# Performance work log

Measured on AMD Instinct MI355X. Metric: run time of the kernel, lower is better.

## Reference

```python
import jax, jax.numpy as jnp
import numpy as np

B, S, D, H, DH = 4, 1024, 1024, 16, 64  # batch, seq, d_model, heads, head dim (d_Q=d_K=d_V)


def setup_inputs() -> dict:
    key = jax.random.key(0)
    ks = jax.random.split(key, 12)
    std = 0.02
    return {
        "x_Q": jax.random.normal(ks[0], (B, S, D), jnp.float32),
        "x_K": jax.random.normal(ks[1], (B, S, D), jnp.float32),
        "x_V": jax.random.normal(ks[2], (B, S, D), jnp.float32),
        "src_batch_lens": jax.random.randint(ks[3], (B,), 0, S),
        # stacked per-head projection weights: [H, d_model, head_dim]
        "Wq": jax.random.normal(ks[4], (H, D, DH), jnp.float32) * std,
        "bq": jax.random.normal(ks[5], (H, DH), jnp.float32) * std,
        "Wk": jax.random.normal(ks[6], (H, D, DH), jnp.float32) * std,
        "bk": jax.random.normal(ks[7], (H, DH), jnp.float32) * std,
        "Wv": jax.random.normal(ks[8], (H, D, DH), jnp.float32) * std,
        "bv": jax.random.normal(ks[9], (H, DH), jnp.float32) * std,
        "Wo": jax.random.normal(ks[10], (D, D), jnp.float32) * std,
        "bo": jax.random.normal(ks[11], (D,), jnp.float32) * std,
    }


def reference(x_Q, x_K, x_V, src_batch_lens, Wq, bq, Wk, bk, Wv, bv, Wo, bo):
    dq = Wq.shape[-1]
    seq = x_Q.shape[1]
    # all heads at once instead of the per-head python loop
    Q = jnp.einsum('bsd,hde->bhse', x_Q, Wq) + bq[None, :, None, :]
    K = jnp.einsum('bsd,hde->bhse', x_K, Wk) + bk[None, :, None, :]
    V = jnp.einsum('bsd,hde->bhse', x_V, Wv) + bv[None, :, None, :]
    scores = jnp.einsum('bhse,bhte->bhst', Q, K) / jnp.sqrt(jnp.asarray(dq, x_Q.dtype))
    # original: matmul(diag(1..1,0..0), scores) zeroes query rows >= length
    rowmask = (jnp.arange(seq)[None, :] < src_batch_lens[:, None])  # [B, S]
    scores = scores * rowmask[:, None, :, None].astype(scores.dtype)
    A = jax.nn.softmax(scores, axis=-1)  # torch Softmax(dim=2) on [B,S,S] per head = key axis
    AV = jnp.einsum('bhst,bhtv->bhsv', A, V)
    out = AV.transpose(0, 2, 1, 3).reshape(x_Q.shape[0], seq, -1)  # concat heads on dim 2
    return out @ Wo + bo  # dropout p=0 -> identity
```

## Files before the change

### kernel.cpp

```cpp
#include <hip/hip_runtime.h>
#include <stdint.h>

typedef short v8s __attribute__((ext_vector_type(8)));
typedef short v4s __attribute__((ext_vector_type(4)));
typedef float v4f __attribute__((ext_vector_type(4)));

#define AS1 __attribute__((address_space(1)))
#define AS3 __attribute__((address_space(3)))

__device__ __forceinline__ void glds16(const void* g, void* l) {
  __builtin_amdgcn_global_load_lds((const AS1 void*)g, (AS3 void*)l, 16, 0, 0);
}

__device__ __forceinline__ short f2bf(float f) {
  uint32_t u = __float_as_uint(f);
  u += 0x7fffu + ((u >> 16) & 1u);
  return (short)(u >> 16);
}

__global__ __launch_bounds__(256) void prep_kernel(
    const float* __restrict__ xQ, const float* __restrict__ xK, const float* __restrict__ xV,
    const float* __restrict__ wq, const float* __restrict__ wk, const float* __restrict__ wv,
    const float* __restrict__ wo,
    short* __restrict__ oxQ, short* __restrict__ oxK, short* __restrict__ oxV,
    short* __restrict__ oq, short* __restrict__ ok, short* __restrict__ ov,
    short* __restrict__ oo) {
  const int bid = blockIdx.x;
  const int t = threadIdx.x;
  if (bid >= 1024) {
    const int c = bid - 1024;
    const int z = c >> 12;
    const int i = (c & 4095) * 256 + t;
    const float* in = (z == 0) ? xQ : (z == 1) ? xK : xV;
    short* out      = (z == 0) ? oxQ : (z == 1) ? oxK : oxV;
    float4 v = ((const float4*)in)[i];
    short4 o = { f2bf(v.x), f2bf(v.y), f2bf(v.z), f2bf(v.w) };
    ((short4*)out)[i] = o;
    return;
  }
  __shared__ float tile[64][65];
  const float* in;
  short* out;
  int C, R, rb, cb;
  if (bid < 768) {
    const int which = bid >> 8, rem = bid & 255;
    const int slice = rem >> 4, rbi = rem & 15;
    in  = ((which == 0) ? wq : (which == 1) ? wk : wv) + (size_t)slice * 65536;
    out = ((which == 0) ? oq : (which == 1) ? ok : ov) + (size_t)slice * 65536;
    C = 64; R = 1024; rb = rbi * 64; cb = 0;
  } else {
    const int r = bid - 768;
    in = wo; out = oo;
    C = 1024; R = 1024; rb = (r >> 4) * 64; cb = (r & 15) * 64;
  }
  const int col = t & 63, r0 = t >> 6;
#pragma unroll
  for (int i = 0; i < 16; ++i) {
    int row = r0 + i * 4;
    tile[row][col] = in[(size_t)(rb + row) * C + cb + col];
  }
  __syncthreads();
#pragma unroll
  for (int i = 0; i < 16; ++i) {
    int orow = r0 + i * 4;
    out[(size_t)(cb + orow) * R + rb + col] = f2bf(tile[col][orow]);
  }
}

template <int MR>
__device__ __forceinline__ void gemm_core(const short* __restrict__ Ag,
                                          const short* __restrict__ Bg,
                                          short* As, short* Bs,
                                          v4f (&acc)[MR / 32][4]) {
  constexpr int MT = MR / 32;
  constexpr int ASZ = MR * 32;
  constexpr int BSZ = 128 * 32;
  const int tid  = threadIdx.x;
  const int lane = tid & 63;
  const int w    = tid >> 6;
  const int quad = lane >> 4;
  const int c15  = lane & 15;
  const int wr   = (w >> 1) * (MR / 2);
  const int wc   = (w & 1) * 64;

  const int r0 = tid >> 2;
  const int p0 = (tid & 3) ^ ((r0 & 3) ^ ((r0 >> 2) & 3));
  const short* a0 = Ag + (size_t)r0 * 1024 + p0 * 8;
  const short* a1 = a0 + 64 * 1024;
  const short* b0 = Bg + (size_t)r0 * 1024 + p0 * 8;
  const short* b1 = b0 + 64 * 1024;
  short* lA = As + tid * 8;
  short* lB = Bs + tid * 8;

  auto issue = [&](int t, int buf) {
    const int o = t * 32;
    glds16(a0 + o, lA + buf * ASZ);
    if constexpr (MR == 128) glds16(a1 + o, lA + buf * ASZ + 2048);
    glds16(b0 + o, lB + buf * BSZ);
    glds16(b1 + o, lB + buf * BSZ + 2048);
  };

  issue(0, 0);
  issue(1, 1);

  const int xs = (c15 & 3) ^ ((c15 >> 2) & 3);
  const int rdoff = ((quad ^ xs)) * 8;

  for (int kb = 0; kb < 32; ++kb) {
    if constexpr (MR == 128)
      asm volatile("s_waitcnt vmcnt(4)\n\ts_barrier" ::: "memory");
    else
      asm volatile("s_waitcnt vmcnt(3)\n\ts_barrier" ::: "memory");

    const int t2 = kb + 2;
    issue(t2 < 32 ? t2 : 31, t2 % 3);

    const short* Ab = As + (kb % 3) * ASZ;
    const short* Bb = Bs + (kb % 3) * BSZ;

    v8s a[MT], b[4];
#pragma unroll
    for (int mt = 0; mt < MT; ++mt)
      a[mt] = *(const v8s*)(Ab + (wr + mt * 16 + c15) * 32 + rdoff);
#pragma unroll
    for (int nt = 0; nt < 4; ++nt)
      b[nt] = *(const v8s*)(Bb + (wc + nt * 16 + c15) * 32 + rdoff);
#pragma unroll
    for (int mt = 0; mt < MT; ++mt)
#pragma unroll
      for (int nt = 0; nt < 4; ++nt)
        acc[mt][nt] = __builtin_amdgcn_mfma_f32_16x16x32_bf16(a[mt], b[nt], acc[mt][nt], 0, 0, 0);
  }
}

__global__ __launch_bounds__(256, 3) void proj_gemm(
    const short* __restrict__ xQ, const short* __restrict__ xK, const short* __restrict__ xV,
    const short* __restrict__ WqT, const short* __restrict__ WkT, const short* __restrict__ WvT,
    const float* __restrict__ bq, const float* __restrict__ bk, const float* __restrict__ bv,
    short* __restrict__ Qb, short* __restrict__ Kb, short* __restrict__ Vtb) {
  __shared__ short As[12288];
  __shared__ short Bs[12288];
  const int lin = blockIdx.x;
  const int z = lin >> 8;
  const int r = lin & 255;
  const int nb = ((r >> 3) & 7) * 128;
  const int mb = (((r & 7) << 2) + (r >> 6)) * 128;
  const short* A    = (z == 0) ? xQ  : (z == 1) ? xK  : xV;
  const short* Bt   = (z == 0) ? WqT : (z == 1) ? WkT : WvT;
  const float* bias = (z == 0) ? bq  : (z == 1) ? bk  : bv;
  short* outp       = (z == 0) ? Qb  : (z == 1) ? Kb  : Vtb;
  v4f acc[4][4] = {};
  gemm_core<128>(A + (size_t)mb * 1024, Bt + (size_t)nb * 1024, As, Bs, acc);

  const int lane = threadIdx.x & 63, w = threadIdx.x >> 6;
  const int quad = lane >> 4, c15 = lane & 15;
  const int wr = (w >> 1) * 64, wc = (w & 1) * 64;
  const bool vmode = (z == 2);
#pragma unroll
  for (int nt = 0; nt < 4; ++nt) {
    const int gn = nb + wc + nt * 16 + c15;
    const float bb = bias[gn];
    const int h = gn >> 6, e = gn & 63;
#pragma unroll
    for (int mt = 0; mt < 4; ++mt) {
      if (!vmode) {
#pragma unroll
        for (int rr = 0; rr < 4; ++rr) {
          const int gm = mb + wr + mt * 16 + quad * 4 + rr;
          const int bi = gm >> 10, s = gm & 1023;
          const size_t base = (size_t)(bi * 16 + h) * 65536;
          outp[base + (size_t)s * 64 + e] = f2bf(acc[mt][nt][rr] + bb);
        }
      } else {
        const int gm0 = mb + wr + mt * 16 + quad * 4;
        const int bi = gm0 >> 10, s0 = gm0 & 1023;
        const size_t base = (size_t)(bi * 16 + h) * 65536;
        short4 st = { f2bf(acc[mt][nt][0] + bb), f2bf(acc[mt][nt][1] + bb),
                      f2bf(acc[mt][nt][2] + bb), f2bf(acc[mt][nt][3] + bb) };
        *(short4*)&outp[base + (size_t)e * 1024 + s0] = st;
      }
    }
  }
}

__global__ __launch_bounds__(256, 3) void out_gemm(
    const short* __restrict__ AV, const short* __restrict__ WoT,
    const float* __restrict__ bo, float* __restrict__ outp) {
  __shared__ short As[6144];
  __shared__ short Bs[12288];
  const int lin = blockIdx.x;
  const int nb = ((lin >> 3) & 7) * 128;
  const int mb = (((lin & 7) << 3) + (lin >> 6)) * 64;
  v4f acc[2][4] = {};
  gemm_core<64>(AV + (size_t)mb * 1024, WoT + (size_t)nb * 1024, As, Bs, acc);
  const int lane = threadIdx.x & 63, w = threadIdx.x >> 6;
  const int quad = lane >> 4, c15 = lane & 15;
  const int wr = (w >> 1) * 32, wc = (w & 1) * 64;
#pragma unroll
  for (int nt = 0; nt < 4; ++nt) {
    const int gn = nb + wc + nt * 16 + c15;
    const float bb = bo[gn];
#pragma unroll
    for (int mt = 0; mt < 2; ++mt)
#pragma unroll
      for (int r = 0; r < 4; ++r) {
        const int gm = mb + wr + mt * 16 + quad * 4 + r;
        outp[(size_t)gm * 1024 + gn] = acc[mt][nt][r] + bb;
      }
  }
}

__global__ __launch_bounds__(256, 4) void attn_kernel(
    const short* __restrict__ Qb, const short* __restrict__ Kb,
    const short* __restrict__ Vtb, const int* __restrict__ lens,
    short* __restrict__ AVb) {
  __shared__ short Ks[2][4096];
  __shared__ short Vs[2][4096];
  const int tid = threadIdx.x, lane = tid & 63, w = tid >> 6;
  const int quad = lane >> 4, c15 = lane & 15;
  const int flat = blockIdx.x;
  const int bh = (flat & 7) + 8 * ((flat >> 3) & 7);
  const int qg = flat >> 6;
  const int b = bh >> 4, h = bh & 15;
  const short* Qp = Qb  + (size_t)bh * 65536;
  const short* Kp = Kb  + (size_t)bh * 65536;
  const short* Vp = Vtb + (size_t)bh * 65536;
  const int len = lens[b];
  const int row0 = qg * 64 + w * 16;

  v8s bq_[2];
#pragma unroll
  for (int kf = 0; kf < 2; ++kf)
    bq_[kf] = *(const v8s*)(Qp + (size_t)(row0 + c15) * 64 + kf * 32 + quad * 8);

  const float scale = (row0 + c15 < len) ? 0.125f : 0.0f;
  float sm = 0.f;
  v4f o[4] = {};

  const int srow = tid >> 3, spart = tid & 7;
  const int gpart = spart ^ (srow & 7);
  const int kgo0 = srow * 64 + gpart * 8, kgo1 = (srow + 32) * 64 + gpart * 8;
  const int vgo0 = srow * 1024 + gpart * 8, vgo1 = (srow + 32) * 1024 + gpart * 8;
  const int l0 = tid * 8, l1 = 2048 + tid * 8;

  const int c7 = c15 & 7;
  const int krow = c15 * 128;
  const int koff0 = krow + ((quad) ^ c7) * 16;
  const int koff1 = krow + ((4 + quad) ^ c7) * 16;
  const int q2 = quad >> 1, h8 = (quad & 1) * 8;
  int voff[4];
#pragma unroll
  for (int nt = 0; nt < 4; ++nt)
    voff[nt] = krow + ((2 * nt + q2) ^ c7) * 16 + h8;

  glds16(Kp + kgo0, (char*)Ks[0] + l0 * 2);
  glds16(Kp + kgo1, (char*)Ks[0] + l1 * 2);
  glds16(Vp + vgo0, (char*)Vs[0] + l0 * 2);
  glds16(Vp + vgo1, (char*)Vs[0] + l1 * 2);

  for (int kb = 0; kb < 16; ++kb) {
    const int cur = kb & 1, nxt = cur ^ 1;
    __syncthreads();

    if (kb < 15) {
      const short* kt = Kp + (size_t)(kb + 1) * 4096;
      const short* vt = Vp + (kb + 1) * 64;
      glds16(kt + kgo0, (char*)Ks[nxt] + l0 * 2);
      glds16(kt + kgo1, (char*)Ks[nxt] + l1 * 2);
      glds16(vt + vgo0, (char*)Vs[nxt] + l0 * 2);
      glds16(vt + vgo1, (char*)Vs[nxt] + l1 * 2);
    }

    v8s ak[4][2];
#pragma unroll
    for (int nt = 0; nt < 4; ++nt) {
      ak[nt][0] = *(const v8s*)((const char*)Ks[cur] + nt * 2048 + koff0);
      ak[nt][1] = *(const v8s*)((const char*)Ks[cur] + nt * 2048 + koff1);
    }

    v4f sc[4];
#pragma unroll
    for (int nt = 0; nt < 4; ++nt) {
      v4f z = {};
#pragma unroll
      for (int kf = 0; kf < 2; ++kf)
        z = __builtin_amdgcn_mfma_f32_16x16x32_bf16(ak[nt][kf], bq_[kf], z, 0, 0, 0);
      sc[nt] = z;
    }

    v4s pb[4];
#pragma unroll
    for (int nt = 0; nt < 4; ++nt) {
      v4s pv;
#pragma unroll
      for (int r = 0; r < 4; ++r) {
        float p = __expf(sc[nt][r] * scale);
        sm += p;
        pv[r] = f2bf(p);
      }
      pb[nt] = pv;
    }

    v4s av[4][4];
#pragma unroll
    for (int t = 0; t < 4; ++t)
#pragma unroll
      for (int nt = 0; nt < 4; ++nt)
        av[t][nt] = *(const v4s*)((const char*)Vs[cur] + t * 2048 + voff[nt]);

#pragma unroll
    for (int t = 0; t < 4; ++t)
#pragma unroll
      for (int nt = 0; nt < 4; ++nt)
        o[t] = __builtin_amdgcn_mfma_f32_16x16x16bf16_1k(av[t][nt], pb[nt], o[t], 0, 0, 0);
  }

  sm += __shfl_xor(sm, 16);
  sm += __shfl_xor(sm, 32);

  const float inv = 1.0f / sm;
  const size_t rowbase = (size_t)(b * 1024 + row0 + c15) * 1024 + h * 64;
#pragma unroll
  for (int t = 0; t < 4; ++t) {
    short4 st = { f2bf(o[t][0] * inv), f2bf(o[t][1] * inv),
                  f2bf(o[t][2] * inv), f2bf(o[t][3] * inv) };
    *(short4*)&AVb[rowbase + t * 16 + quad * 4] = st;
  }
}

extern "C" void kernel_launch(void* const* d_in, const int* in_sizes, int n_in,
                              void* d_out, int out_size, void* d_ws, size_t ws_size,
                              hipStream_t stream) {
  const float* xQ = (const float*)d_in[0];
  const float* xK = (const float*)d_in[1];
  const float* xV = (const float*)d_in[2];
  const int* lens = (const int*)d_in[3];
  const float* Wq = (const float*)d_in[4];
  const float* bq = (const float*)d_in[5];
  const float* Wk = (const float*)d_in[6];
  const float* bk = (const float*)d_in[7];
  const float* Wv = (const float*)d_in[8];
  const float* bv = (const float*)d_in[9];
  const float* Wo = (const float*)d_in[10];
  const float* bo = (const float*)d_in[11];
  float* out = (float*)d_out;

  char* ws = (char*)d_ws;
  short* xQb = (short*)(ws + 0);
  short* xKb = (short*)(ws + 8388608);
  short* xVb = (short*)(ws + 16777216);
  short* WqT = (short*)(ws + 25165824);
  short* WkT = (short*)(ws + 27262976);
  short* WvT = (short*)(ws + 29360128);
  short* WoT = (short*)(ws + 31457280);
  short* Qb  = (short*)(ws + 33554432);
  short* Kb  = (short*)(ws + 41943040);
  short* Vtb = (short*)(ws + 50331648);
  short* AVb = (short*)(ws + 58720256);

  prep_kernel<<<dim3(13312), 256, 0, stream>>>(xQ, xK, xV, Wq, Wk, Wv, Wo,
                                               xQb, xKb, xVb, WqT, WkT, WvT, WoT);
  proj_gemm<<<dim3(768), 256, 0, stream>>>(xQb, xKb, xVb, WqT, WkT, WvT,
                                           bq, bk, bv, Qb, Kb, Vtb);
  attn_kernel<<<dim3(1024), 256, 0, stream>>>(Qb, Kb, Vtb, lens, AVb);
  out_gemm<<<dim3(512), 256, 0, stream>>>(AVb, WoT, bo, out);
}
```

Before: 202.5 us.

## Rewrite projection GEMM with 256x256 tiles, 8 waves and double-buffered swizzled LDS

The QKV projection GEMM moves from 128x128 tiles with 4 waves to 256x256 tiles with 8 waves per block (192 blocks instead of 768). It uses double-buffered LDS with XOR-swizzled columns and K-step 64, and issues async global-to-LDS loads staged across four compute phases with explicit barriers and s_setprio around the MFMA bursts. The aim is more data reuse per byte loaded and better overlap of memory with compute. The risks are fewer blocks than CUs on the chip and higher register and LDS pressure.

New measurement: 207.5 us. +2.4%, slower.

```diff
diff --git a/kernel.cpp b/kernel.cpp
--- a/kernel.cpp
+++ b/kernel.cpp
@@ -133,46 +133,133 @@
   }
 }
 
-__global__ __launch_bounds__(256, 3) void proj_gemm(
+#define MFMA16(A, B, C) __builtin_amdgcn_mfma_f32_16x16x32_bf16(A, B, C, 0, 0, 0)
+
+__global__ __launch_bounds__(512, 2) void proj_gemm(
     const short* __restrict__ xQ, const short* __restrict__ xK, const short* __restrict__ xV,
     const short* __restrict__ WqT, const short* __restrict__ WkT, const short* __restrict__ WvT,
     const float* __restrict__ bq, const float* __restrict__ bk, const float* __restrict__ bv,
     short* __restrict__ Qb, short* __restrict__ Kb, short* __restrict__ Vtb) {
-  __shared__ short As[12288];
-  __shared__ short Bs[12288];
+  __shared__ short As_[2][16384];
+  __shared__ short Bs_[2][16384];
+
   const int lin = blockIdx.x;
-  const int z = lin >> 8;
-  const int r = lin & 255;
-  const int nb = ((r >> 3) & 7) * 128;
-  const int mb = (((r & 7) << 2) + (r >> 6)) * 128;
-  const short* A    = (z == 0) ? xQ  : (z == 1) ? xK  : xV;
-  const short* Bt   = (z == 0) ? WqT : (z == 1) ? WkT : WvT;
+  const int z = lin >> 6;
+  const int r6 = lin & 63;
+  const int tile = (r6 & 7) * 8 + (r6 >> 3);
+  const int mbase = (tile >> 2) * 256;
+  const int nbase = (tile & 3) * 256;
+
+  const short* Ag   = (z == 0) ? xQ  : (z == 1) ? xK  : xV;
+  const short* Bg   = (z == 0) ? WqT : (z == 1) ? WkT : WvT;
   const float* bias = (z == 0) ? bq  : (z == 1) ? bk  : bv;
   short* outp       = (z == 0) ? Qb  : (z == 1) ? Kb  : Vtb;
-  v4f acc[4][4] = {};
-  gemm_core<128>(A + (size_t)mb * 1024, Bt + (size_t)nb * 1024, As, Bs, acc);
-
-  const int lane = threadIdx.x & 63, w = threadIdx.x >> 6;
+
+  const int tid  = threadIdx.x;
+  const int lane = tid & 63, w = tid >> 6;
+  const int wm = w >> 2, wn = w & 3;
   const int quad = lane >> 4, c15 = lane & 15;
-  const int wr = (w >> 1) * 64, wc = (w & 1) * 64;
+  const int g3 = c15 & 7;
+  const int off0 = (quad ^ g3) * 8;
+  const int off1 = ((4 | quad) ^ g3) * 8;
+
+  const int sr = tid >> 3, sl = tid & 7;
+  const int scol = (sl ^ (sr & 7)) << 3;
+
+  auto stage = [&](int q_) {
+    if (q_ >= 128) return;
+    const int T = q_ >> 3, k = q_ & 7, bf = T & 1;
+    if (k < 4) {
+      glds16(Bg + (size_t)(nbase + k * 64 + sr) * 1024 + T * 64 + scol,
+             &Bs_[bf][k * 4096 + tid * 8]);
+    } else {
+      const int q = k - 4;
+      const int lrow = q * 32 + sr + ((sr & 32) ? 96 : 0);
+      glds16(Ag + (size_t)(mbase + lrow) * 1024 + T * 64 + scol,
+             &As_[bf][lrow * 64 + sl * 8]);
+    }
+  };
+
+  for (int i = 0; i < 11; ++i) stage(i);
+  int rq = 11;
+
+  v4f acc[8][4] = {};
+
+  asm volatile("s_waitcnt vmcnt(3)\n\ts_barrier" ::: "memory");
+
+#pragma unroll 2
+  for (int t = 0; t < 16; ++t) {
+    const short* pA = &As_[t & 1][(wm * 128 + c15) * 64];
+    const short* pB = &Bs_[t & 1][(wn * 64 + c15) * 64];
+    v8s a[2][2], b[4][2];
+
+#pragma unroll
+    for (int nf = 0; nf < 4; ++nf) {
+      b[nf][0] = *(const v8s*)(pB + nf * 1024 + off0);
+      b[nf][1] = *(const v8s*)(pB + nf * 1024 + off1);
+    }
+    a[0][0] = *(const v8s*)(pA + off0);
+    a[0][1] = *(const v8s*)(pA + off1);
+    a[1][0] = *(const v8s*)(pA + 1024 + off0);
+    a[1][1] = *(const v8s*)(pA + 1024 + off1);
+    stage(rq); stage(rq + 1); rq += 2;
+    asm volatile("s_barrier" ::: "memory");
+    __builtin_amdgcn_s_setprio(1);
+#pragma unroll
+    for (int mf = 0; mf < 2; ++mf)
+#pragma unroll
+      for (int nf = 0; nf < 4; ++nf)
+        acc[mf][nf] = MFMA16(a[mf][1], b[nf][1], MFMA16(a[mf][0], b[nf][0], acc[mf][nf]));
+    __builtin_amdgcn_s_setprio(0);
+    asm volatile("s_barrier" ::: "memory");
+
+#define PROJ_PHASE(P)                                                         \
+    a[0][0] = *(const v8s*)(pA + (P) * 2048 + off0);                          \
+    a[0][1] = *(const v8s*)(pA + (P) * 2048 + off1);                          \
+    a[1][0] = *(const v8s*)(pA + (P) * 2048 + 1024 + off0);                   \
+    a[1][1] = *(const v8s*)(pA + (P) * 2048 + 1024 + off1);                   \
+    stage(rq); stage(rq + 1); rq += 2;                                        \
+    asm volatile("s_barrier" ::: "memory");                                   \
+    __builtin_amdgcn_s_setprio(1);                                            \
+    _Pragma("unroll")                                                         \
+    for (int mf = 0; mf < 2; ++mf)                                            \
+      _Pragma("unroll")                                                       \
+      for (int nf = 0; nf < 4; ++nf)                                          \
+        acc[(P) * 2 + mf][nf] =                                               \
+            MFMA16(a[mf][1], b[nf][1],                                        \
+                   MFMA16(a[mf][0], b[nf][0], acc[(P) * 2 + mf][nf]));        \
+    __builtin_amdgcn_s_setprio(0);
+
+    PROJ_PHASE(1)
+    asm volatile("s_barrier" ::: "memory");
+    PROJ_PHASE(2)
+    asm volatile("s_barrier" ::: "memory");
+    PROJ_PHASE(3)
+    if (t < 14)
+      asm volatile("s_waitcnt vmcnt(3)\n\ts_barrier" ::: "memory");
+    else if (t == 14)
+      asm volatile("s_waitcnt vmcnt(0)\n\ts_barrier" ::: "memory");
+  }
+#undef PROJ_PHASE
+
   const bool vmode = (z == 2);
 #pragma unroll
   for (int nt = 0; nt < 4; ++nt) {
-    const int gn = nb + wc + nt * 16 + c15;
+    const int gn = nbase + wn * 64 + nt * 16 + c15;
     const float bb = bias[gn];
     const int h = gn >> 6, e = gn & 63;
 #pragma unroll
-    for (int mt = 0; mt < 4; ++mt) {
+    for (int mt = 0; mt < 8; ++mt) {
       if (!vmode) {
 #pragma unroll
         for (int rr = 0; rr < 4; ++rr) {
-          const int gm = mb + wr + mt * 16 + quad * 4 + rr;
+          const int gm = mbase + wm * 128 + mt * 16 + quad * 4 + rr;
           const int bi = gm >> 10, s = gm & 1023;
           const size_t base = (size_t)(bi * 16 + h) * 65536;
           outp[base + (size_t)s * 64 + e] = f2bf(acc[mt][nt][rr] + bb);
         }
       } else {
-        const int gm0 = mb + wr + mt * 16 + quad * 4;
+        const int gm0 = mbase + wm * 128 + mt * 16 + quad * 4;
         const int bi = gm0 >> 10, s0 = gm0 & 1023;
         const size_t base = (size_t)(bi * 16 + h) * 65536;
         short4 st = { f2bf(acc[mt][nt][0] + bb), f2bf(acc[mt][nt][1] + bb),
@@ -360,7 +447,7 @@
 
   prep_kernel<<<dim3(13312), 256, 0, stream>>>(xQ, xK, xV, Wq, Wk, Wv, Wo,
                                                xQb, xKb, xVb, WqT, WkT, WvT, WoT);
-  proj_gemm<<<dim3(768), 256, 0, stream>>>(xQb, xKb, xVb, WqT, WkT, WvT,
+  proj_gemm<<<dim3(192), 512, 0, stream>>>(xQb, xKb, xVb, WqT, WkT, WvT,
                                            bq, bk, bv, Qb, Kb, Vtb);
   attn_kernel<<<dim3(1024), 256, 0, stream>>>(Qb, Kb, Vtb, lens, AVb);
   out_gemm<<<dim3(512), 256, 0, stream>>>(AVb, WoT, bo, out);
```

## Process two query tiles per warp in attention to reuse K/V LDS fragments

Applied to the files above, without the earlier changes.

Each warp in the attention kernel now handles 32 query rows instead of 16, so every K and V fragment read from shared memory feeds two MFMA streams. Each block covers 128 query rows, and the grid is halved to 512 blocks. The intent is to cut LDS traffic and global K/V tile loads per query row. The cost is doubled accumulator and score registers, a lower occupancy target (launch bounds 2), and fewer blocks for latency hiding across the GPU's compute units.

After: 203.2 us. About the same (+0.3%).

```diff
diff --git a/kernel.cpp b/kernel.cpp
--- a/kernel.cpp
+++ b/kernel.cpp
@@ -210,7 +210,7 @@
   }
 }
 
-__global__ __launch_bounds__(256, 4) void attn_kernel(
+__global__ __launch_bounds__(256, 2) void attn_kernel(
     const short* __restrict__ Qb, const short* __restrict__ Kb,
     const short* __restrict__ Vtb, const int* __restrict__ lens,
     short* __restrict__ AVb) {
@@ -226,16 +226,20 @@
   const short* Kp = Kb  + (size_t)bh * 65536;
   const short* Vp = Vtb + (size_t)bh * 65536;
   const int len = lens[b];
-  const int row0 = qg * 64 + w * 16;
-
-  v8s bq_[2];
-#pragma unroll
-  for (int kf = 0; kf < 2; ++kf)
-    bq_[kf] = *(const v8s*)(Qp + (size_t)(row0 + c15) * 64 + kf * 32 + quad * 8);
-
-  const float scale = (row0 + c15 < len) ? 0.125f : 0.0f;
-  float sm = 0.f;
-  v4f o[4] = {};
+  const int row0 = qg * 128 + w * 32;
+
+  v8s bq_[2][2];
+#pragma unroll
+  for (int qf = 0; qf < 2; ++qf)
+#pragma unroll
+    for (int kf = 0; kf < 2; ++kf)
+      bq_[qf][kf] = *(const v8s*)(Qp + (size_t)(row0 + qf * 16 + c15) * 64 + kf * 32 + quad * 8);
+
+  float scale[2];
+  scale[0] = (row0 + c15 < len) ? 0.125f : 0.0f;
+  scale[1] = (row0 + 16 + c15 < len) ? 0.125f : 0.0f;
+  float sm[2] = {0.f, 0.f};
+  v4f o[2][4] = {};
 
   const int srow = tid >> 3, spart = tid & 7;
   const int gpart = spart ^ (srow & 7);
@@ -278,28 +282,32 @@
       ak[nt][1] = *(const v8s*)((const char*)Ks[cur] + nt * 2048 + koff1);
     }
 
-    v4f sc[4];
-#pragma unroll
-    for (int nt = 0; nt < 4; ++nt) {
-      v4f z = {};
-#pragma unroll
-      for (int kf = 0; kf < 2; ++kf)
-        z = __builtin_amdgcn_mfma_f32_16x16x32_bf16(ak[nt][kf], bq_[kf], z, 0, 0, 0);
-      sc[nt] = z;
-    }
-
-    v4s pb[4];
-#pragma unroll
-    for (int nt = 0; nt < 4; ++nt) {
-      v4s pv;
-#pragma unroll
-      for (int r = 0; r < 4; ++r) {
-        float p = __expf(sc[nt][r] * scale);
-        sm += p;
-        pv[r] = f2bf(p);
-      }
-      pb[nt] = pv;
-    }
+    v4f sc[2][4];
+#pragma unroll
+    for (int qf = 0; qf < 2; ++qf)
+#pragma unroll
+      for (int nt = 0; nt < 4; ++nt) {
+        v4f z = {};
+#pragma unroll
+        for (int kf = 0; kf < 2; ++kf)
+          z = __builtin_amdgcn_mfma_f32_16x16x32_bf16(ak[nt][kf], bq_[qf][kf], z, 0, 0, 0);
+        sc[qf][nt] = z;
+      }
+
+    v4s pb[2][4];
+#pragma unroll
+    for (int qf = 0; qf < 2; ++qf)
+#pragma unroll
+      for (int nt = 0; nt < 4; ++nt) {
+        v4s pv;
+#pragma unroll
+        for (int r = 0; r < 4; ++r) {
+          float p = __expf(sc[qf][nt][r] * scale[qf]);
+          sm[qf] += p;
+          pv[r] = f2bf(p);
+        }
+        pb[qf][nt] = pv;
+      }
 
     v4s av[4][4];
 #pragma unroll
@@ -311,20 +319,25 @@
 #pragma unroll
     for (int t = 0; t < 4; ++t)
 #pragma unroll
-      for (int nt = 0; nt < 4; ++nt)
-        o[t] = __builtin_amdgcn_mfma_f32_16x16x16bf16_1k(av[t][nt], pb[nt], o[t], 0, 0, 0);
-  }
-
-  sm += __shfl_xor(sm, 16);
-  sm += __shfl_xor(sm, 32);
-
-  const float inv = 1.0f / sm;
-  const size_t rowbase = (size_t)(b * 1024 + row0 + c15) * 1024 + h * 64;
-#pragma unroll
-  for (int t = 0; t < 4; ++t) {
-    short4 st = { f2bf(o[t][0] * inv), f2bf(o[t][1] * inv),
-                  f2bf(o[t][2] * inv), f2bf(o[t][3] * inv) };
-    *(short4*)&AVb[rowbase + t * 16 + quad * 4] = st;
+      for (int nt = 0; nt < 4; ++nt) {
+        o[0][t] = __builtin_amdgcn_mfma_f32_16x16x16bf16_1k(av[t][nt], pb[0][nt], o[0][t], 0, 0, 0);
+        o[1][t] = __builtin_amdgcn_mfma_f32_16x16x16bf16_1k(av[t][nt], pb[1][nt], o[1][t], 0, 0, 0);
+      }
+  }
+
+#pragma unroll
+  for (int qf = 0; qf < 2; ++qf) {
+    float s = sm[qf];
+    s += __shfl_xor(s, 16);
+    s += __shfl_xor(s, 32);
+    const float inv = 1.0f / s;
+    const size_t rowbase = (size_t)(b * 1024 + row0 + qf * 16 + c15) * 1024 + h * 64;
+#pragma unroll
+    for (int t = 0; t < 4; ++t) {
+      short4 st = { f2bf(o[qf][t][0] * inv), f2bf(o[qf][t][1] * inv),
+                    f2bf(o[qf][t][2] * inv), f2bf(o[qf][t][3] * inv) };
+      *(short4*)&AVb[rowbase + t * 16 + quad * 4] = st;
+    }
   }
 }
 
@@ -362,6 +375,6 @@
                                                xQb, xKb, xVb, WqT, WkT, WvT, WoT);
   proj_gemm<<<dim3(768), 256, 0, stream>>>(xQb, xKb, xVb, WqT, WkT, WvT,
                                            bq, bk, bv, Qb, Kb, Vtb);
-  attn_kernel<<<dim3(1024), 256, 0, stream>>>(Qb, Kb, Vtb, lens, AVb);
+  attn_kernel<<<dim3(512), 256, 0, stream>>>(Qb, Kb, Vtb, lens, AVb);
   out_gemm<<<dim3(512), 256, 0, stream>>>(AVb, WoT, bo, out);
 }
```
